# Kernel optimization log

Measured on AMD Instinct MI355X. Metric: run time of the kernel, lower is better.

## Reference

```python
import jax, jax.numpy as jnp
import numpy as np

B, S, D, H = 4, 2048, 1024, 16
HD = D // H


def setup_inputs() -> dict:
    key = jax.random.key(0)
    ks = jax.random.split(key, 5)
    scale = 1.0 / np.sqrt(D)
    return {
        "x": jax.random.normal(ks[0], (B, S, D), dtype=jnp.float32),
        "W_q": jax.random.normal(ks[1], (D, D), dtype=jnp.float32) * scale,
        "W_k": jax.random.normal(ks[2], (D, D), dtype=jnp.float32) * scale,
        "W_v": jax.random.normal(ks[3], (D, D), dtype=jnp.float32) * scale,
        "W_o": jax.random.normal(ks[4], (D, D), dtype=jnp.float32) * scale,
    }


def reference(x, W_q, W_k, W_v, W_o):
    # Linear with weight [out, in]: y = x @ W^T
    def proj(W):
        return jnp.einsum('bsd,ed->bshf', x, W.reshape(H, HD, D).transpose(0, 1, 2).reshape(D, D)) if False else (x @ W.T).reshape(B, S, H, HD).transpose(0, 2, 1, 3)

    q = proj(W_q)  # [B, H, S, HD]
    k = proj(W_k)
    v = proj(W_v)

    scores = jnp.einsum('bhqd,bhkd->bhqk', q, k) / jnp.sqrt(jnp.float32(HD))
    causal = jnp.triu(jnp.ones((S, S), dtype=bool), k=1)  # True above diagonal -> masked
    scores = jnp.where(causal, -jnp.inf, scores)
    probs = jax.nn.softmax(scores, axis=-1)
    out = jnp.einsum('bhqk,bhkd->bhqd', probs, v)  # [B, H, S, HD]
    out = out.transpose(0, 2, 1, 3).reshape(B, S, D)
    return out @ W_o.T
```

## Files before the change

### kernel.cpp

```cpp
#include <hip/hip_runtime.h>
#include <cstdint>
#include <cstddef>

typedef unsigned short u16;
typedef __attribute__((ext_vector_type(8))) short short8;
typedef __attribute__((ext_vector_type(4))) short short4v;
typedef __attribute__((ext_vector_type(8))) unsigned short ushort8v;
typedef __attribute__((ext_vector_type(4))) unsigned short ushort4v;
typedef __attribute__((ext_vector_type(4))) unsigned int uint4v;
typedef __attribute__((ext_vector_type(4))) float f32x4;

#define QSCALE 0.18033688011112042f
#define THR_L2 11.5417f


__device__ __forceinline__ u16 f2bf(float f) {
  unsigned int u = __builtin_bit_cast(unsigned int, f);
  u += 0x7FFFu + ((u >> 16) & 1u);
  return (u16)(u >> 16);
}

__device__ __forceinline__ void async16(const void* g, void* l) {
  __builtin_amdgcn_global_load_lds(
      (const __attribute__((address_space(1))) unsigned int*)g,
      (__attribute__((address_space(3))) unsigned int*)l, 16, 0, 0);
}

__device__ __forceinline__ float fmax3(float a, float b, float c) {
  float r;
  asm("v_max3_f32 %0, %1, %2, %3" : "=v"(r) : "v"(a), "v"(b), "v"(c));
  return r;
}

__device__ __forceinline__ unsigned int cvtpk(float lo, float hi) {
  unsigned int r;
  asm("v_cvt_pk_bf16_f32 %0, %1, %2" : "=v"(r) : "v"(lo), "v"(hi));
  return r;
}


__global__ void cvt_all(const float* __restrict__ x, const float* __restrict__ Wq,
                        const float* __restrict__ Wk, const float* __restrict__ Wv,
                        const float* __restrict__ Wo, u16* __restrict__ out) {
  const int bid = blockIdx.x;
  const float* src;
  int i;
  size_t doff;
  if (bid < 8192) {
    i = bid * 1024 + threadIdx.x * 4;
    src = x;
    doff = (size_t)i;
  } else {
    const int k = bid - 8192;
    const int wsel = k >> 10;
    i = (k & 1023) * 1024 + threadIdx.x * 4;
    src = (wsel == 0) ? Wq : (wsel == 1) ? Wk : (wsel == 2) ? Wv : Wo;
    doff = 8388608 + (size_t)wsel * 1048576 + i;
  }
  float4 v = *(const float4*)(src + i);
  ushort4v o;
  o[0] = f2bf(v.x); o[1] = f2bf(v.y); o[2] = f2bf(v.z); o[3] = f2bf(v.w);
  *(ushort4v*)(out + doff) = o;
}


template<int MODE>
__global__ __launch_bounds__(512, 4) void gemm_tb(
    const u16* __restrict__ A, const u16* __restrict__ Bw,
    void* __restrict__ Cout, int M, int N, int K)
{
  const int t = threadIdx.x;
  const int lane = t & 63, w = t >> 6;
  const int li = lane & 15, g = lane >> 4;
  const int wm = w >> 1, wn = w & 1;

  const int nx = gridDim.x;
  const int hwid = blockIdx.y * nx + blockIdx.x;
  const int cpx = (nx * gridDim.y) >> 3;
  const int lid = (hwid & 7) * cpx + (hwid >> 3);
  const int brow = (lid / nx) * 256, bcol = (lid % nx) * 128;

  __shared__ u16 As[3][256 * 32];
  __shared__ u16 Bs[3][128 * 32];

  f32x4 acc[4][4];
#pragma unroll
  for (int i = 0; i < 4; ++i)
#pragma unroll
    for (int j = 0; j < 4; ++j) acc[i][j] = f32x4{0.f, 0.f, 0.f, 0.f};

  auto STAGE = [&](int T) {
    const int b = T % 3;
    const int k0 = T * 32;
#pragma unroll
    for (int L = 0; L < 2; ++L) {
      const int f2 = t + 512 * L;
      const int row = f2 >> 2;
      const int cb = ((f2 & 3) * 16) ^ (((row >> 1) & 3) << 4);
      async16(A + (size_t)(brow + row) * K + k0 + (cb >> 1), &As[b][f2 * 8]);
    }
    const int rowb = t >> 2;
    const int cbb = ((t & 3) * 16) ^ (((rowb >> 1) & 3) << 4);
    async16(Bw + (size_t)(bcol + rowb) * K + k0 + (cbb >> 1), &Bs[b][t * 8]);
  };

  STAGE(0); STAGE(1);

  const int NT = K >> 5;
  const int ksw = (g * 8) ^ (((li >> 1) & 3) << 3);

#pragma unroll 1
  for (int T = 0; T < NT; ++T) {
    if (T < NT - 1) asm volatile("s_waitcnt vmcnt(3)" ::: "memory");
    else            asm volatile("s_waitcnt vmcnt(0)" ::: "memory");
    asm volatile("s_barrier" ::: "memory");
    const int b = T % 3;
    short8 af[4], bfr[4];
#pragma unroll
    for (int mt = 0; mt < 4; ++mt)
      af[mt] = *(const short8*)&As[b][(wm * 64 + mt * 16 + li) * 32 + ksw];
#pragma unroll
    for (int nt = 0; nt < 4; ++nt)
      bfr[nt] = *(const short8*)&Bs[b][(wn * 64 + nt * 16 + li) * 32 + ksw];

    if (T + 2 < NT) STAGE(T + 2);

    __builtin_amdgcn_s_setprio(1);
#pragma unroll
    for (int mt = 0; mt < 4; ++mt)
#pragma unroll
      for (int nt = 0; nt < 4; ++nt)
        acc[mt][nt] = __builtin_amdgcn_mfma_f32_16x16x32_bf16(af[mt], bfr[nt], acc[mt][nt], 0, 0, 0);
    __builtin_amdgcn_s_setprio(0);
  }

#pragma unroll
  for (int mt = 0; mt < 4; ++mt)
#pragma unroll
    for (int nt = 0; nt < 4; ++nt) {
      const int col = bcol + wn * 64 + nt * 16 + li;
      const int row0 = brow + wm * 64 + mt * 16 + g * 4;
      if (MODE == 1) {
#pragma unroll
        for (int r = 0; r < 4; ++r)
          ((float*)Cout)[(size_t)(row0 + r) * N + col] = acc[mt][nt][r];
      } else {
        const int which = col >> 10;
        const int c2 = col & 1023;
        const int h = c2 >> 6, hd = c2 & 63;
        const int bb = row0 >> 11, s0 = row0 & 2047;
        if (which == 2) {
          const int kv = s0 & 63;
          const int pos = (kv & 0x23) | ((kv & 0x10) >> 2) | ((kv & 0x0C) << 1);
          ushort4v st;
#pragma unroll
          for (int r = 0; r < 4; ++r) st[r] = f2bf(acc[mt][nt][r]);
          *(ushort4v*)((u16*)Cout + (size_t)3 * 8388608 +
                       (size_t)(bb * 16 + h) * 131072 + (size_t)hd * 2048 +
                       (s0 >> 6) * 64 + pos) = st;
        } else {
#pragma unroll
          for (int r = 0; r < 4; ++r) {
            float v = acc[mt][nt][r];
            if (which == 0) v *= QSCALE;
            ((u16*)Cout)[(size_t)which * 8388608 +
                         (((size_t)(bb * 16 + h) * 2048) + s0 + r) * 64 + hd] = f2bf(v);
          }
        }
      }
    }
}


__global__ __launch_bounds__(256, 4) void flash_attn11(
    const u16* __restrict__ Qp, const u16* __restrict__ Kp,
    const u16* __restrict__ VTp, u16* __restrict__ Oattn)
{
  const int id = blockIdx.x;
  const int c = id & 255, k = id >> 8;
  const int bh = (c & 7) * 8 + (c >> 5);
  const int r4 = (c >> 3) & 3;
  const int base = 2 * r4 + (k >> 1);
  const int p = (k & 1) ? 15 - base : base;
  const int qbase = p * 128;
  const int njb = 2 * p + 2;

  const int t = threadIdx.x;
  const int lane = t & 63, w = t >> 6;
  const int li = lane & 15, g = lane >> 4;

  __shared__ u16 Kl[2][64 * 64];
  __shared__ u16 Vl[2][64 * 64];

  const size_t bh_off = (size_t)bh * (2048 * 64);
  const int b = bh >> 4, h = bh & 15;
  const int ksw = (li & 7) << 3;

  short8 qc[2][2];
#pragma unroll
  for (int qs = 0; qs < 2; ++qs) {
    const u16* qp = Qp + bh_off + (size_t)(qbase + qs * 64 + w * 16 + li) * 64 + g * 8;
    qc[qs][0] = *(const short8*)qp;
    qc[qs][1] = *(const short8*)(qp + 32);
  }

  short8 onesf;
#pragma unroll
  for (int j = 0; j < 8; ++j) onesf[j] = (short)0x3F80;

  f32x4 o_acc[2][4];
  f32x4 osum[2];
#pragma unroll
  for (int qs = 0; qs < 2; ++qs) {
    osum[qs] = f32x4{0.f, 0.f, 0.f, 0.f};
#pragma unroll
    for (int i = 0; i < 4; ++i) o_acc[qs][i] = f32x4{0.f, 0.f, 0.f, 0.f};
  }
  float m_i[2] = {-1e30f, -1e30f};

  auto STAGE = [&](int jb, int s) {
#pragma unroll
    for (int L = 0; L < 2; ++L) {
      const int f = t + 256 * L;
      const int kbyte = (f * 16) ^ (((f >> 3) & 7) << 4);
      async16(Kp + bh_off + (size_t)jb * 4096 + (kbyte >> 1),
              &Kl[s][(w * 64 + 256 * L) * 8]);
      const int vrow = f >> 3;
      const int vb = ((f & 7) * 16) ^ ((vrow & 7) << 4);
      async16(VTp + bh_off + (size_t)vrow * 2048 + jb * 64 + (vb >> 1),
              &Vl[s][(w * 64 + 256 * L) * 8]);
    }
  };

  STAGE(0, 0);
  asm volatile("s_waitcnt vmcnt(0)" ::: "memory");
  __builtin_amdgcn_s_barrier();

#pragma unroll 1
  for (int i = 0; i < njb; ++i) {
    const int s = i & 1;
    if (i + 1 < njb) STAGE(i + 1, (i + 1) & 1);

    const int jb = i;
    const u16* __restrict__ Ks = &Kl[s][0];
    const u16* __restrict__ Vs = &Vl[s][0];

    f32x4 s_acc[2][4];
#pragma unroll
    for (int qs = 0; qs < 2; ++qs)
#pragma unroll
      for (int jt = 0; jt < 4; ++jt) s_acc[qs][jt] = f32x4{0.f, 0.f, 0.f, 0.f};
    __builtin_amdgcn_s_setprio(1);
#pragma unroll
    for (int kc = 0; kc < 2; ++kc)
#pragma unroll
      for (int jt = 0; jt < 4; ++jt) {
        short8 kf = *(const short8*)&Ks[(jt * 16 + li) * 64 + ((kc * 32 + g * 8) ^ ksw)];
        s_acc[0][jt] = __builtin_amdgcn_mfma_f32_16x16x32_bf16(kf, qc[0][kc], s_acc[0][jt], 0, 0, 0);
        s_acc[1][jt] = __builtin_amdgcn_mfma_f32_16x16x32_bf16(kf, qc[1][kc], s_acc[1][jt], 0, 0, 0);
      }
    __builtin_amdgcn_s_setprio(0);

    float mx[2];
    bool need = false;
#pragma unroll
    for (int qs = 0; qs < 2; ++qs) {
      if (jb * 64 + 63 > qbase + qs * 64 + w * 16) {
        const int tq = qbase + qs * 64 + w * 16 + li - jb * 64;
#pragma unroll
        for (int jt = 0; jt < 4; ++jt)
#pragma unroll
          for (int r = 0; r < 4; ++r)
            if (jt * 16 + g * 4 + r > tq) s_acc[qs][jt][r] = -1e30f;
      }
      float t0 = fmax3(s_acc[qs][0][0], s_acc[qs][0][1], s_acc[qs][0][2]);
      float t1 = fmax3(s_acc[qs][0][3], s_acc[qs][1][0], s_acc[qs][1][1]);
      float t2 = fmax3(s_acc[qs][1][2], s_acc[qs][1][3], s_acc[qs][2][0]);
      float t3 = fmax3(s_acc[qs][2][1], s_acc[qs][2][2], s_acc[qs][2][3]);
      float t4m = fmax3(s_acc[qs][3][0], s_acc[qs][3][1], s_acc[qs][3][2]);
      float m01 = fmax3(t0, t1, s_acc[qs][3][3]);
      float m23 = fmax3(t2, t3, t4m);
      float mm = fmaxf(m01, m23);
      mm = fmaxf(mm, __shfl_xor(mm, 16));
      mm = fmaxf(mm, __shfl_xor(mm, 32));
      mx[qs] = mm;
      need = need || (mm > m_i[qs] + THR_L2);
    }

    if (__any((int)need)) {
#pragma unroll
      for (int qs = 0; qs < 2; ++qs) {
        const float mn = fmaxf(m_i[qs], mx[qs]);
        const float corr = __builtin_amdgcn_exp2f(m_i[qs] - mn);
        osum[qs] *= corr;
#pragma unroll
        for (int dt = 0; dt < 4; ++dt) o_acc[qs][dt] *= corr;
        m_i[qs] = mn;
      }
    }

    short8 pf[2][2];
#pragma unroll
    for (int qs = 0; qs < 2; ++qs) {
      const float mi = m_i[qs];
#pragma unroll
      for (int jt = 0; jt < 4; ++jt)
#pragma unroll
        for (int r = 0; r < 4; ++r)
          s_acc[qs][jt][r] = __builtin_amdgcn_exp2f(s_acc[qs][jt][r] - mi);
#pragma unroll
      for (int kc = 0; kc < 2; ++kc) {
        uint4v u;
        u[0] = cvtpk(s_acc[qs][2 * kc][0], s_acc[qs][2 * kc][1]);
        u[1] = cvtpk(s_acc[qs][2 * kc][2], s_acc[qs][2 * kc][3]);
        u[2] = cvtpk(s_acc[qs][2 * kc + 1][0], s_acc[qs][2 * kc + 1][1]);
        u[3] = cvtpk(s_acc[qs][2 * kc + 1][2], s_acc[qs][2 * kc + 1][3]);
        pf[qs][kc] = __builtin_bit_cast(short8, u);
      }
    }

    __builtin_amdgcn_s_setprio(1);
#pragma unroll
    for (int kc = 0; kc < 2; ++kc) {
      osum[0] = __builtin_amdgcn_mfma_f32_16x16x32_bf16(onesf, pf[0][kc], osum[0], 0, 0, 0);
      osum[1] = __builtin_amdgcn_mfma_f32_16x16x32_bf16(onesf, pf[1][kc], osum[1], 0, 0, 0);
#pragma unroll
      for (int dt = 0; dt < 4; ++dt) {
        short8 vf = *(const short8*)&Vs[(dt * 16 + li) * 64 + ((kc * 32 + g * 8) ^ ksw)];
        o_acc[0][dt] = __builtin_amdgcn_mfma_f32_16x16x32_bf16(vf, pf[0][kc], o_acc[0][dt], 0, 0, 0);
        o_acc[1][dt] = __builtin_amdgcn_mfma_f32_16x16x32_bf16(vf, pf[1][kc], o_acc[1][dt], 0, 0, 0);
      }
    }
    __builtin_amdgcn_s_setprio(0);

    asm volatile("s_waitcnt lgkmcnt(0)" ::: "memory");
    asm volatile("s_waitcnt vmcnt(0)" ::: "memory");
    __builtin_amdgcn_s_barrier();
  }

#pragma unroll
  for (int qs = 0; qs < 2; ++qs) {
    const float inv_l = 1.f / osum[qs][0];
    const int qrow = qbase + qs * 64 + w * 16 + li;
    u16* op = Oattn + ((size_t)(b * 2048 + qrow)) * 1024 + h * 64;
#pragma unroll
    for (int dt = 0; dt < 4; ++dt) {
      ushort4v st;
#pragma unroll
      for (int r = 0; r < 4; ++r) st[r] = f2bf(o_acc[qs][dt][r] * inv_l);
      *(ushort4v*)(op + dt * 16 + g * 4) = st;
    }
  }
}


extern "C" void kernel_launch(void* const* d_in, const int* in_sizes, int n_in,
                              void* d_out, int out_size, void* d_ws, size_t ws_size,
                              hipStream_t stream) {
  const float* x  = (const float*)d_in[0];
  const float* Wq = (const float*)d_in[1];
  const float* Wk = (const float*)d_in[2];
  const float* Wv = (const float*)d_in[3];
  const float* Wo = (const float*)d_in[4];

  const size_t NX = 8388608;
  const size_t NW = 1048576;

  u16* xb  = (u16*)d_ws;
  u16* wqb = xb + NX;
  u16* wob = wqb + 3 * NW;
  u16* Qb  = wob + NW;
  u16* Kb  = Qb + NX;
  u16* VTb = Qb + 3 * NX;
  u16* attnb = Qb + 2 * NX;

  cvt_all<<<12288, 256, 0, stream>>>(x, Wq, Wk, Wv, Wo, xb);

  gemm_tb<0><<<dim3(24, 32), 512, 0, stream>>>(xb, wqb, Qb, 8192, 3072, 1024);

  flash_attn11<<<1024, 256, 0, stream>>>(Qb, Kb, VTb, attnb);

  gemm_tb<1><<<dim3(8, 32), 512, 0, stream>>>(attnb, wob, d_out, 8192, 1024, 1024);
}
```

Measured before the change: 150.9 us.

## Replace QKV projection GEMM with 256x256-tile, 8-phase double-buffered kernel

Adds a new QKV projection GEMM that uses 256x256 output tiles with K-step 64, XOR-swizzled LDS, and a double buffer. Each K-tile is split into four phases, with barriers between phases and next-tile prefetches interleaved into the first two. The larger tile raises arithmetic intensity per LDS load, so fewer loads are needed per MFMA. In exchange, occupancy drops to one block per CU and the grid shrinks to 384 blocks, which may leave CUs imbalanced. The old templated GEMM now has only the fp32 output path.

```diff
diff --git a/kernel.cpp b/kernel.cpp
--- a/kernel.cpp
+++ b/kernel.cpp
@@ -64,6 +64,126 @@
 }
 
 
+__global__ __launch_bounds__(512, 1) void gemm_8p(
+    const u16* __restrict__ A, const u16* __restrict__ Bw,
+    u16* __restrict__ Cout, int M, int N, int K)
+{
+  const int t = threadIdx.x;
+  const int lane = t & 63, w = t >> 6;
+  const int li = lane & 15, g = lane >> 4;
+  const int wm = w >> 2, wn = w & 3;
+
+  const int nx = gridDim.x;
+  const int hwid = blockIdx.y * nx + blockIdx.x;
+  const int cpx = (nx * gridDim.y) >> 3;
+  const int lid = (hwid & 7) * cpx + (hwid >> 3);
+  const int brow = (lid / nx) * 256, bcol = (lid % nx) * 256;
+
+  __shared__ u16 As[2][256 * 64];
+  __shared__ u16 Bs[2][256 * 64];
+
+  f32x4 acc[8][4];
+#pragma unroll
+  for (int i = 0; i < 8; ++i)
+#pragma unroll
+    for (int j = 0; j < 4; ++j) acc[i][j] = f32x4{0.f, 0.f, 0.f, 0.f};
+
+  auto STAGE2 = [&](int kt, int p) {
+    const int nb = kt & 1;
+    const int k0 = kt * 64;
+#pragma unroll
+    for (int q = 0; q < 2; ++q) {
+      const int f = t + 512 * (2 * p + q);
+      const int row = f >> 3;
+      const int ce = ((f & 7) ^ (row & 7)) * 8;
+      async16(A + (size_t)(brow + row) * K + k0 + ce, &As[nb][f * 8]);
+      async16(Bw + (size_t)(bcol + row) * K + k0 + ce, &Bs[nb][f * 8]);
+    }
+  };
+
+  STAGE2(0, 0); STAGE2(0, 1);
+  asm volatile("s_waitcnt vmcnt(0)" ::: "memory");
+  __builtin_amdgcn_s_barrier();
+
+  const int nkt = K >> 6;
+  const int asw = (li & 7) << 3;
+
+#pragma unroll 1
+  for (int kt = 0; kt < nkt; ++kt) {
+    const u16* __restrict__ Ab = &As[kt & 1][0];
+    const u16* __restrict__ Bb = &Bs[kt & 1][0];
+    short8 bfr[4][2];
+#pragma unroll
+    for (int p = 0; p < 4; ++p) {
+      if (p == 0) {
+#pragma unroll
+        for (int nf = 0; nf < 4; ++nf)
+#pragma unroll
+          for (int ks = 0; ks < 2; ++ks)
+            bfr[nf][ks] = *(const short8*)&Bb[(wn * 64 + nf * 16 + li) * 64 +
+                                             ((ks * 32 + g * 8) ^ asw)];
+      }
+      short8 af[2][2];
+#pragma unroll
+      for (int ai = 0; ai < 2; ++ai)
+#pragma unroll
+        for (int ks = 0; ks < 2; ++ks)
+          af[ai][ks] = *(const short8*)&Ab[(wm * 128 + (p * 2 + ai) * 16 + li) * 64 +
+                                           ((ks * 32 + g * 8) ^ asw)];
+      if (p < 2 && kt + 1 < nkt) STAGE2(kt + 1, p);
+
+      __builtin_amdgcn_s_setprio(1);
+#pragma unroll
+      for (int ai = 0; ai < 2; ++ai)
+#pragma unroll
+        for (int nf = 0; nf < 4; ++nf)
+#pragma unroll
+          for (int ks = 0; ks < 2; ++ks)
+            acc[p * 2 + ai][nf] = __builtin_amdgcn_mfma_f32_16x16x32_bf16(
+                af[ai][ks], bfr[nf][ks], acc[p * 2 + ai][nf], 0, 0, 0);
+      __builtin_amdgcn_s_setprio(0);
+
+      if (p < 3) {
+        __builtin_amdgcn_s_barrier();
+      } else if (kt + 1 < nkt) {
+        asm volatile("s_waitcnt vmcnt(0)" ::: "memory");
+        __builtin_amdgcn_s_barrier();
+      }
+    }
+  }
+
+#pragma unroll
+  for (int mf = 0; mf < 8; ++mf)
+#pragma unroll
+    for (int nf = 0; nf < 4; ++nf) {
+      const int col = bcol + wn * 64 + nf * 16 + li;
+      const int row0 = brow + wm * 128 + mf * 16 + g * 4;
+      const int which = col >> 10;
+      const int c2 = col & 1023;
+      const int h = c2 >> 6, hd = c2 & 63;
+      const int bb = row0 >> 11, s0 = row0 & 2047;
+      if (which == 2) {
+        const int kv = s0 & 63;
+        const int pos = (kv & 0x23) | ((kv & 0x10) >> 2) | ((kv & 0x0C) << 1);
+        ushort4v st;
+#pragma unroll
+        for (int r = 0; r < 4; ++r) st[r] = f2bf(acc[mf][nf][r]);
+        *(ushort4v*)(Cout + (size_t)3 * 8388608 +
+                     (size_t)(bb * 16 + h) * 131072 + (size_t)hd * 2048 +
+                     (s0 >> 6) * 64 + pos) = st;
+      } else {
+#pragma unroll
+        for (int r = 0; r < 4; ++r) {
+          float v = acc[mf][nf][r];
+          if (which == 0) v *= QSCALE;
+          Cout[(size_t)which * 8388608 +
+               (((size_t)(bb * 16 + h) * 2048) + s0 + r) * 64 + hd] = f2bf(v);
+        }
+      }
+    }
+}
+
+
 template<int MODE>
 __global__ __launch_bounds__(512, 4) void gemm_tb(
     const u16* __restrict__ A, const u16* __restrict__ Bw,
@@ -140,34 +260,9 @@
     for (int nt = 0; nt < 4; ++nt) {
       const int col = bcol + wn * 64 + nt * 16 + li;
       const int row0 = brow + wm * 64 + mt * 16 + g * 4;
-      if (MODE == 1) {
-#pragma unroll
-        for (int r = 0; r < 4; ++r)
-          ((float*)Cout)[(size_t)(row0 + r) * N + col] = acc[mt][nt][r];
-      } else {
-        const int which = col >> 10;
-        const int c2 = col & 1023;
-        const int h = c2 >> 6, hd = c2 & 63;
-        const int bb = row0 >> 11, s0 = row0 & 2047;
-        if (which == 2) {
-          const int kv = s0 & 63;
-          const int pos = (kv & 0x23) | ((kv & 0x10) >> 2) | ((kv & 0x0C) << 1);
-          ushort4v st;
-#pragma unroll
-          for (int r = 0; r < 4; ++r) st[r] = f2bf(acc[mt][nt][r]);
-          *(ushort4v*)((u16*)Cout + (size_t)3 * 8388608 +
-                       (size_t)(bb * 16 + h) * 131072 + (size_t)hd * 2048 +
-                       (s0 >> 6) * 64 + pos) = st;
-        } else {
-#pragma unroll
-          for (int r = 0; r < 4; ++r) {
-            float v = acc[mt][nt][r];
-            if (which == 0) v *= QSCALE;
-            ((u16*)Cout)[(size_t)which * 8388608 +
-                         (((size_t)(bb * 16 + h) * 2048) + s0 + r) * 64 + hd] = f2bf(v);
-          }
-        }
-      }
+#pragma unroll
+      for (int r = 0; r < 4; ++r)
+        ((float*)Cout)[(size_t)(row0 + r) * N + col] = acc[mt][nt][r];
     }
 }
 
@@ -376,7 +471,7 @@
 
   cvt_all<<<12288, 256, 0, stream>>>(x, Wq, Wk, Wv, Wo, xb);
 
-  gemm_tb<0><<<dim3(24, 32), 512, 0, stream>>>(xb, wqb, Qb, 8192, 3072, 1024);
+  gemm_8p<<<dim3(12, 32), 512, 0, stream>>>(xb, wqb, Qb, 8192, 3072, 1024);
 
   flash_attn11<<<1024, 256, 0, stream>>>(Qb, Kb, VTb, attnb);
 
```

New measurement: 158.9 us. +5.3%, slower.
